# Optimization experiments

Measured on AMD Instinct MI355X. Metric: run time of the kernel, lower is better.

## Reference

```python
import jax, jax.numpy as jnp
import numpy as np

N_USERS = 100000
N_ITEMS = 50000
DIM = 64
HID = 64
E = 3200000
B = 16384


def setup_inputs() -> dict:
    key = jax.random.key(0)
    ks = jax.random.split(key, 16)
    N = N_USERS + N_ITEMS
    return {
        "users": jax.random.randint(ks[0], (B,), 0, N_USERS),
        "items": jax.random.randint(ks[1], (B,), 0, N_ITEMS),
        "edge_index": jax.random.randint(ks[2], (2, E), 0, N),
        "edge_weight": jax.random.uniform(ks[3], (E,), dtype=jnp.float32),
        # learned parameters
        "U": jax.random.normal(ks[4], (N_USERS, DIM), jnp.float32) * 0.1,
        "I": jax.random.normal(ks[5], (N_ITEMS, DIM), jnp.float32) * 0.1,
        "W0": jax.random.normal(ks[6], (DIM, HID), jnp.float32) / np.sqrt(DIM),
        "b0": jnp.zeros((HID,), jnp.float32),
        "g0": jnp.ones((HID,), jnp.float32),
        "be0": jnp.zeros((HID,), jnp.float32),
        "W1": jax.random.normal(ks[7], (HID, HID), jnp.float32) / np.sqrt(HID),
        "b1": jnp.zeros((HID,), jnp.float32),
        "g1": jnp.ones((HID,), jnp.float32),
        "be1": jnp.zeros((HID,), jnp.float32),
        "Wp": jax.random.normal(ks[8], (HID, DIM), jnp.float32) / np.sqrt(HID),
        "bp": jnp.zeros((DIM,), jnp.float32),
        "bu": jnp.zeros((N_USERS,), jnp.float32),
        "bi": jnp.zeros((N_ITEMS,), jnp.float32),
        "mu": jnp.zeros((), jnp.float32),
    }


def _layernorm(h, g, b, eps=1e-5):
    m = jnp.mean(h, axis=-1, keepdims=True)
    v = jnp.mean(jnp.square(h - m), axis=-1, keepdims=True)
    return (h - m) * jax.lax.rsqrt(v + eps) * g + b


def reference(users, items, edge_index, edge_weight, U, I,
              W0, b0, g0, be0, W1, b1, g1, be1, Wp, bp, bu, bi, mu):
    N = U.shape[0] + I.shape[0]
    x = jnp.concatenate([U, I], axis=0)  # [N, DIM]

    # GCN normalization with added self-loops (torch_geometric gcn_norm)
    loop = jnp.arange(N)
    src = jnp.concatenate([edge_index[0], loop])
    dst = jnp.concatenate([edge_index[1], loop])
    ew = jnp.concatenate([edge_weight, jnp.ones((N,), edge_weight.dtype)])
    deg = jax.ops.segment_sum(ew, dst, num_segments=N)
    dinv = jnp.where(deg > 0, jax.lax.rsqrt(deg), 0.0)
    norm = dinv[src] * ew * dinv[dst]  # [E+N]

    def conv(h, W, b):
        hw = h @ W  # [N, HID]
        msgs = norm[:, None] * hw[src]  # gather: [E+N, HID]
        return jax.ops.segment_sum(msgs, dst, num_segments=N) + b

    # layer 0: conv -> layernorm -> relu -> (dropout=identity, eval) -> residual
    h = x
    h_in = h
    h = conv(h, W0, b0)
    h = jax.nn.relu(_layernorm(h, g0, be0)) + h_in
    # layer 1
    h_in = h
    h = conv(h, W1, b1)
    h = jax.nn.relu(_layernorm(h, g1, be1)) + h_in

    h = h @ Wp + bp  # proj_out: [N, DIM]
    h_user = h[:U.shape[0]]
    h_item = h[U.shape[0]:]

    s = jnp.sum(h_user[users] * h_item[items], axis=-1)
    s = s + bu[users] + bi[items] + mu
    return jnp.clip(s, 1.0, 5.0)
```

## Files before the change

kernel.cpp:

```cpp
#include <hip/hip_runtime.h>

#define NU 100000
#define NI 50000
#define NN 150000
#define D  64
#define CAP 47
#define OVF_MAX 4096

#define BINSHIFT 8
#define BINW 256
#define NBINS 586
#define BINCAP 5848
#define STAGE_CAP 12
#define EPT 4
#define SPILL_CAP 262144

typedef unsigned int uint;
typedef unsigned short ushort;

__device__ __forceinline__ float half_reduce_add(float v) {
    #pragma unroll
    for (int m = 16; m >= 1; m >>= 1) v += __shfl_xor(v, m, 64);
    return v;
}
__device__ __forceinline__ ushort f2bf(float f) {
    union { float f; uint i; } c; c.f = f;
    uint r = c.i + 0x7FFF + ((c.i >> 16) & 1);
    return (ushort)(r >> 16);
}
__device__ __forceinline__ float bf2f(ushort u) {
    union { uint i; float f; } c; c.i = ((uint)u) << 16; return c.f;
}
__device__ __forceinline__ float bflo(uint u) {
    return __int_as_float((int)(u << 16));
}
__device__ __forceinline__ float bfhi(uint u) {
    return __int_as_float((int)(u & 0xFFFF0000u));
}
__device__ __forceinline__ uint packbf2(float a, float b) {
    return (uint)f2bf(a) | ((uint)f2bf(b) << 16);
}
__device__ __forceinline__ float lane_bcast(float v, int l) {
    return __int_as_float(__builtin_amdgcn_readlane(__float_as_int(v), l));
}
__device__ __forceinline__ uint enc14(float w) {
    uint b = __float_as_uint(w) + 0x00020000u;
    return b & 0xFFFC0000u;
}
__device__ __forceinline__ float dec14(uint r) {
    return __uint_as_float(r & 0xFFFC0000u);
}
__device__ __forceinline__ uint enc6(float w) {
    int q = (int)(w * 64.0f);
    return (uint)(q < 0 ? 0 : (q > 63 ? 63 : q));
}
__device__ __forceinline__ float dec6(uint q) {
    return ((float)q + 0.5f) * (1.0f / 64.0f);
}
__device__ __forceinline__ void spill_one(int d, uint s, float w,
        uint2* __restrict__ spill, int* __restrict__ spillcnt) {
    int si = atomicAdd(spillcnt, 1);
    if (si < SPILL_CAP) spill[si] = make_uint2(s | enc14(w), (uint)d);
}

__global__ __launch_bounds__(256) void k_bin(
        const int* __restrict__ src, const int* __restrict__ dst,
        const float* __restrict__ ew, int* __restrict__ bincur,
        uint* __restrict__ binbuf, uint2* __restrict__ spill,
        int* __restrict__ spillcnt, int E) {
    __shared__ uint stage[NBINS][STAGE_CAP];
    __shared__ int scnt[NBINS];
    int t = threadIdx.x;
    for (int i = t; i < NBINS; i += 256) scnt[i] = 0;
    __syncthreads();
    const int batch = 256 * EPT;
    for (int base = blockIdx.x * batch; base < E; base += gridDim.x * batch) {
        int dd[EPT]; uint ss[EPT]; float ww[EPT]; int ok[EPT];
        #pragma unroll
        for (int k = 0; k < EPT; ++k) {
            int e = base + k * 256 + t;
            ok[k] = (e < E);
            if (ok[k]) { dd[k] = dst[e]; ss[k] = (uint)src[e]; ww[k] = ew[e]; }
        }
        #pragma unroll
        for (int k = 0; k < EPT; ++k) {
            if (!ok[k]) continue;
            int bin = dd[k] >> BINSHIFT;
            int slot = atomicAdd(&scnt[bin], 1);
            if (slot < STAGE_CAP) {
                stage[bin][slot] = ss[k]
                    | ((uint)(dd[k] & (BINW - 1)) << 18)
                    | (enc6(ww[k]) << 26);
            } else {
                spill_one(dd[k], ss[k], ww[k], spill, spillcnt);
            }
        }
        __syncthreads();
        for (int bin = t; bin < NBINS; bin += 256) {
            int c = scnt[bin]; if (c > STAGE_CAP) c = STAGE_CAP;
            while (c >= 8) {
                int b0 = atomicAdd(&bincur[bin], 8);
                if (b0 + 8 <= BINCAP) {
                    uint4* o4 = (uint4*)(binbuf + (size_t)bin * BINCAP + b0);
                    uint* s1 = &stage[bin][c - 8];
                    o4[0] = make_uint4(s1[0], s1[1], s1[2], s1[3]);
                    o4[1] = make_uint4(s1[4], s1[5], s1[6], s1[7]);
                } else {
                    for (int j = 0; j < 8; ++j) {
                        uint r = stage[bin][c - 8 + j];
                        spill_one((bin << BINSHIFT) + (int)((r >> 18) & 0xFFu),
                                  r & 0x3FFFFu, dec6(r >> 26),
                                  spill, spillcnt);
                    }
                }
                c -= 8;
            }
            scnt[bin] = c;
        }
        __syncthreads();
    }
    for (int bin = t; bin < NBINS; bin += 256) {
        int c = scnt[bin]; if (c > STAGE_CAP) c = STAGE_CAP;
        if (c > 0) {
            int b0 = atomicAdd(&bincur[bin], c);
            for (int j = 0; j < c; ++j) {
                uint r = stage[bin][j];
                if (b0 + j < BINCAP) binbuf[(size_t)bin * BINCAP + b0 + j] = r;
                else spill_one((bin << BINSHIFT) + (int)((r >> 18) & 0xFFu),
                               r & 0x3FFFFu, dec6(r >> 26),
                               spill, spillcnt);
            }
        }
    }
}

__global__ __launch_bounds__(256) void k_regroup(
        const int* __restrict__ bincur, const uint* __restrict__ binbuf,
        const uint2* __restrict__ spill, const int* __restrict__ spillcnt,
        uint* __restrict__ recs, int* __restrict__ cursor,
        float* __restrict__ dinv, int4* __restrict__ ovf,
        int* __restrict__ ovfcnt) {
    __shared__ uint image[256 * CAP];
    __shared__ int cnt[256];
    __shared__ float ovfw[256];
    int t = threadIdx.x;
    int bin = blockIdx.x;
    cnt[t] = 0; ovfw[t] = 0.0f;
    __syncthreads();
    int dbase = bin << BINSHIFT;
    int nrec = bincur[bin]; if (nrec > BINCAP) nrec = BINCAP;
    const uint* bb = binbuf + (size_t)bin * BINCAP;
    for (int i = t; i < nrec; i += 256) {
        uint r = bb[i];
        int dl = (int)((r >> 18) & 0xFFu);
        int slot = atomicAdd(&cnt[dl], 1);
        uint s = r & 0x3FFFFu;
        float w = dec6(r >> 26);
        if (slot < CAP) image[dl * CAP + slot] = enc14(w) | s;
        else {
            atomicAdd(&ovfw[dl], w);
            int o = atomicAdd(ovfcnt, 1);
            if (o < OVF_MAX)
                ovf[o] = make_int4(dbase + dl, (int)s, __float_as_int(w), 0);
        }
    }
    int ns = spillcnt[0]; if (ns > SPILL_CAP) ns = SPILL_CAP;
    for (int i = t; i < ns; i += 256) {
        uint2 e = spill[i];
        int d = (int)e.y;
        if (d < dbase || d >= dbase + BINW) continue;
        int dl = d - dbase;
        int slot = atomicAdd(&cnt[dl], 1);
        if (slot < CAP) image[dl * CAP + slot] = e.x;
        else {
            float w = dec14(e.x);
            atomicAdd(&ovfw[dl], w);
            int o = atomicAdd(ovfcnt, 1);
            if (o < OVF_MAX) ovf[o] = make_int4(d, (int)(e.x & 0x3FFFFu),
                                                __float_as_int(w), 0);
        }
    }
    __syncthreads();
    int ndl = NN - dbase; if (ndl > 256) ndl = 256;
    if (ndl <= 0) return;
    if (t < ndl) {
        int c = cnt[t];
        cursor[dbase + t] = c;
        if (c > CAP) c = CAP;
        float dg = ovfw[t];
        for (int j = 0; j < c; ++j) dg += dec14(image[t * CAP + j]);
        dinv[dbase + t] = rsqrtf(dg + 1.0f);
    }
    int tot = ndl * CAP;
    uint* out = recs + (size_t)dbase * CAP;
    for (int i = t; i < tot; i += 256) out[i] = image[i];
}

__global__ __launch_bounds__(256) void k_gemm(
        const ushort* __restrict__ h, const float* __restrict__ U,
        const float* __restrict__ I, const float* __restrict__ W,
        const float* __restrict__ dinv, ushort* __restrict__ out) {
    int lane = threadIdx.x & 63;
    float wreg[64];
    #pragma unroll
    for (int k = 0; k < 64; ++k) wreg[k] = W[k * 64 + lane];
    int wpb = blockDim.x >> 6;
    int wid = blockIdx.x * wpb + (threadIdx.x >> 6);
    int tw = gridDim.x * wpb;
    for (int n = wid; n < NN; n += tw) {
        float xv;
        if (h) xv = bf2f(h[(size_t)n * D + lane]);
        else   xv = (n < NU) ? U[(size_t)n * D + lane]
                             : I[(size_t)(n - NU) * D + lane];
        float acc = 0.f;
        #pragma unroll
        for (int k = 0; k < 64; ++k)
            acc = fmaf(lane_bcast(xv, k), wreg[k], acc);
        out[(size_t)n * D + lane] = f2bf(acc * dinv[n]);
    }
}

__device__ __forceinline__ float2 conv_accum2(int n, int lane,
        const uint* __restrict__ hw2p, const int* __restrict__ cursor,
        const uint* __restrict__ recs, const int4* __restrict__ ovf,
        const int* __restrict__ ovfcnt) {
    int cnt = __builtin_amdgcn_readfirstlane(cursor[n]);
    if (cnt > CAP) cnt = CAP;
    uint rv = (lane < cnt) ? recs[(size_t)n * CAP + lane] : 0u;
    int odd = lane >> 5;
    int laneoff = lane & 31;
    float ax = 0.f, ay = 0.f;
    int cp = (cnt + 7) & ~7;
    for (int j0 = 0; j0 < cp; j0 += 8) {
        #pragma unroll
        for (int k = 0; k < 4; ++k) {
            uint re = (uint)__builtin_amdgcn_readlane((int)rv, j0 + 2 * k);
            uint ro = (uint)__builtin_amdgcn_readlane((int)rv, j0 + 2 * k + 1);
            uint r  = odd ? ro : re;
            int   s = (int)(r & 0x3FFFFu);
            float w = dec14(r);
            uint x = hw2p[(size_t)s * 32 + laneoff];
            ax = fmaf(w, bflo(x), ax);
            ay = fmaf(w, bfhi(x), ay);
        }
    }
    ax += __shfl_xor(ax, 32, 64);
    ay += __shfl_xor(ay, 32, 64);
    uint xs = hw2p[(size_t)n * 32 + laneoff];
    ax += bflo(xs);
    ay += bfhi(xs);
    int novf = __builtin_amdgcn_readfirstlane(ovfcnt[0]);
    if (novf > 0) {
        if (novf > OVF_MAX) novf = OVF_MAX;
        for (int j = 0; j < novf; ++j) {
            int4 e = ovf[j];
            if (e.x == n) {
                float w = __int_as_float(e.z);
                uint x = hw2p[(size_t)e.y * 32 + laneoff];
                ax = fmaf(w, bflo(x), ax);
                ay = fmaf(w, bfhi(x), ay);
            }
        }
    }
    return make_float2(ax, ay);
}

__device__ __forceinline__ float2 ln_relu2(float2 a, float di, int p,
        const float* __restrict__ b, const float* __restrict__ g,
        const float* __restrict__ be) {
    float2 bb = ((const float2*)b)[p];
    float v0 = fmaf(a.x, di, bb.x);
    float v1 = fmaf(a.y, di, bb.y);
    float m = half_reduce_add(v0 + v1) * (1.0f / 64.0f);
    float d0 = v0 - m, d1 = v1 - m;
    float var = half_reduce_add(d0 * d0 + d1 * d1) * (1.0f / 64.0f);
    float rs = rsqrtf(var + 1e-5f);
    float2 gg = ((const float2*)g)[p];
    float2 ee = ((const float2*)be)[p];
    return make_float2(fmaxf(fmaf(d0 * rs, gg.x, ee.x), 0.0f),
                       fmaxf(fmaf(d1 * rs, gg.y, ee.y), 0.0f));
}

__global__ __launch_bounds__(256) void k_conv1(
        const uint* __restrict__ hw2p, const int* __restrict__ cursor,
        const uint* __restrict__ recs, const int4* __restrict__ ovf,
        const int* __restrict__ ovfcnt, const float* __restrict__ dinv,
        const float* __restrict__ b, const float* __restrict__ g,
        const float* __restrict__ be, const float* __restrict__ U,
        const float* __restrict__ I, uint* __restrict__ out) {
    int lane = threadIdx.x & 63;
    int n = __builtin_amdgcn_readfirstlane(blockIdx.x * 4 + (threadIdx.x >> 6));
    if (n >= NN) return;
    float2 a = conv_accum2(n, lane, hw2p, cursor, recs, ovf, ovfcnt);
    int p = lane & 31;
    float2 y = ln_relu2(a, dinv[n], p, b, g, be);
    const float* R = (n < NU) ? (U + (size_t)n * D) : (I + (size_t)(n - NU) * D);
    float2 rr = ((const float2*)R)[p];
    if (lane < 32)
        out[(size_t)n * 32 + p] = packbf2(y.x + rr.x, y.y + rr.y);
}

__global__ __launch_bounds__(256) void k_conv2score(
        const uint* __restrict__ hw2p, const int* __restrict__ cursor,
        const uint* __restrict__ recs, const int4* __restrict__ ovf,
        const int* __restrict__ ovfcnt, const float* __restrict__ dinv,
        const float* __restrict__ b, const float* __restrict__ g,
        const float* __restrict__ be, const int* __restrict__ users,
        const int* __restrict__ items, const uint* __restrict__ h1u,
        const float* __restrict__ Wp, const float* __restrict__ bp,
        const float* __restrict__ bu, const float* __restrict__ bi,
        const float* __restrict__ mu, float* __restrict__ out, int B) {
    int lane = threadIdx.x & 63;
    float wreg[64];
    #pragma unroll
    for (int k = 0; k < 64; ++k) wreg[k] = Wp[k * 64 + lane];
    float bpl = bp[lane];
    int q = lane & 31;
    int wpb = blockDim.x >> 6;
    int wid = blockIdx.x * wpb + (threadIdx.x >> 6);
    int tw = gridDim.x * wpb;
    for (int p = wid; p < B; p += tw) {
        int un = users[p];
        int in = NU + items[p];
        int nu = __builtin_amdgcn_readfirstlane(un);
        float2 au = conv_accum2(nu, lane, hw2p, cursor, recs, ovf, ovfcnt);
        float2 yu = ln_relu2(au, dinv[nu], q, b, g, be);
        uint ru = h1u[(size_t)nu * 32 + q];
        float2 hu = make_float2(yu.x + bflo(ru), yu.y + bfhi(ru));
        int ni = __builtin_amdgcn_readfirstlane(in);
        float2 ai = conv_accum2(ni, lane, hw2p, cursor, recs, ovf, ovfcnt);
        float2 yi = ln_relu2(ai, dinv[ni], q, b, g, be);
        uint ri = h1u[(size_t)ni * 32 + q];
        float2 hi = make_float2(yi.x + bflo(ri), yi.y + bfhi(ri));
        float pu = bpl, pi = bpl;
        #pragma unroll
        for (int j = 0; j < 32; ++j) {
            pu = fmaf(lane_bcast(hu.x, j), wreg[2 * j], pu);
            pu = fmaf(lane_bcast(hu.y, j), wreg[2 * j + 1], pu);
            pi = fmaf(lane_bcast(hi.x, j), wreg[2 * j], pi);
            pi = fmaf(lane_bcast(hi.y, j), wreg[2 * j + 1], pi);
        }
        float t = pu * pi;
        #pragma unroll
        for (int m = 32; m >= 1; m >>= 1) t += __shfl_xor(t, m, 64);
        if (lane == 0) {
            t += bu[un] + bi[in - NU] + mu[0];
            out[p] = fminf(fmaxf(t, 1.0f), 5.0f);
        }
    }
}

extern "C" void kernel_launch(void* const* d_in, const int* in_sizes, int n_in,
                              void* d_out, int out_size, void* d_ws, size_t ws_size,
                              hipStream_t stream) {
    const int*   users = (const int*)d_in[0];
    const int*   items = (const int*)d_in[1];
    const int*   ei2   = (const int*)d_in[2];
    const float* ew    = (const float*)d_in[3];
    const float* U     = (const float*)d_in[4];
    const float* I     = (const float*)d_in[5];
    const float* W0    = (const float*)d_in[6];
    const float* b0    = (const float*)d_in[7];
    const float* g0    = (const float*)d_in[8];
    const float* be0   = (const float*)d_in[9];
    const float* W1    = (const float*)d_in[10];
    const float* b1    = (const float*)d_in[11];
    const float* g1    = (const float*)d_in[12];
    const float* be1   = (const float*)d_in[13];
    const float* Wp    = (const float*)d_in[14];
    const float* bp    = (const float*)d_in[15];
    const float* bu    = (const float*)d_in[16];
    const float* bi    = (const float*)d_in[17];
    const float* mu    = (const float*)d_in[18];

    int B = in_sizes[0];
    int E = in_sizes[2] / 2;
    const int* srcp = ei2;
    const int* dstp = ei2 + E;

    char* p = (char*)d_ws;
    auto alloc = [&](size_t bytes) -> char* {
        char* r = p;
        p += (bytes + 255) & ~(size_t)255;
        return r;
    };
    int*    cbuf    = (int*)  alloc((size_t)(NBINS + 8) * 4);
    int*    bincur  = cbuf;
    int*    spillcnt= cbuf + NBINS;
    int*    ovfcnt  = cbuf + NBINS + 1;
    int*    cursor  = (int*)  alloc((size_t)NN * 4);
    float*  dinv    = (float*)alloc((size_t)NN * 4);
    int4*   ovf     = (int4*) alloc((size_t)OVF_MAX * 16);
    char*   regA    = alloc((size_t)NN * D * 2 * 2);
    uint*   binbuf  = (uint*) regA;
    uint2*  spill   = (uint2*)(regA + 16 * 1024 * 1024);
    ushort* hw2b    = (ushort*)regA;
    ushort* h1b     = (ushort*)(regA + (size_t)NN * D * 2);
    uint*   recs    = (uint*) alloc((size_t)NN * CAP * 4);
    const uint* hw2p = (const uint*)hw2b;
    const uint* h1u  = (const uint*)h1b;

    hipMemsetAsync(cbuf, 0, (size_t)(NBINS + 8) * 4, stream);

    int gW = (NN + 3) / 4;

    k_bin<<<768, 256, 0, stream>>>(srcp, dstp, ew, bincur, binbuf,
                                   spill, spillcnt, E);
    k_regroup<<<NBINS, 256, 0, stream>>>(bincur, binbuf, spill, spillcnt,
                                         recs, cursor, dinv, ovf, ovfcnt);

    k_gemm<<<2048, 256, 0, stream>>>(nullptr, U, I, W0, dinv, hw2b);
    k_conv1<<<gW, 256, 0, stream>>>(hw2p, cursor, recs, ovf, ovfcnt, dinv,
                                    b0, g0, be0, U, I, (uint*)h1b);
    k_gemm<<<2048, 256, 0, stream>>>(h1b, U, I, W1, dinv, hw2b);
    k_conv2score<<<1024, 256, 0, stream>>>(hw2p, cursor, recs, ovf, ovfcnt, dinv,
                                           b1, g1, be1, users, items, h1u,
                                           Wp, bp, bu, bi, mu,
                                           (float*)d_out, B);
}
```

Before: 421.6 us.

## Fuse layer GEMMs into regroup and conv1 kernels, dropping standalone GEMM launches

The layer-0 transform (x@W0 scaled by dinv) now runs at the end of the regroup kernel, once each bin's dinv values are known. The layer-1 transform (h1@W1 scaled by dinv) now runs inside conv1 on the freshly computed h1 held in registers. This removes two kernel launches and the re-read of h1 from global memory. It costs extra registers for the weight row in the regroup and conv1 kernels, which may lower occupancy, and it needs separate msg1/msg2 buffers, which changes the workspace layout including where the spill region starts.

```diff
diff --git a/kernel.cpp b/kernel.cpp
--- a/kernel.cpp
+++ b/kernel.cpp
@@ -27,9 +27,6 @@
     union { float f; uint i; } c; c.f = f;
     uint r = c.i + 0x7FFF + ((c.i >> 16) & 1);
     return (ushort)(r >> 16);
-}
-__device__ __forceinline__ float bf2f(ushort u) {
-    union { uint i; float f; } c; c.i = ((uint)u) << 16; return c.f;
 }
 __device__ __forceinline__ float bflo(uint u) {
     return __int_as_float((int)(u << 16));
@@ -134,16 +131,23 @@
     }
 }
 
-__global__ __launch_bounds__(256) void k_regroup(
+__global__ __launch_bounds__(256) void k_regroupg(
         const int* __restrict__ bincur, const uint* __restrict__ binbuf,
         const uint2* __restrict__ spill, const int* __restrict__ spillcnt,
         uint* __restrict__ recs, int* __restrict__ cursor,
         float* __restrict__ dinv, int4* __restrict__ ovf,
-        int* __restrict__ ovfcnt) {
+        int* __restrict__ ovfcnt, const float* __restrict__ U,
+        const float* __restrict__ I, const float* __restrict__ W0,
+        ushort* __restrict__ msg1) {
     __shared__ uint image[256 * CAP];
     __shared__ int cnt[256];
     __shared__ float ovfw[256];
+    __shared__ float sdinv[256];
     int t = threadIdx.x;
+    int lane = t & 63;
+    float wreg[64];
+    #pragma unroll
+    for (int k = 0; k < 64; ++k) wreg[k] = W0[k * 64 + lane];
     int bin = blockIdx.x;
     cnt[t] = 0; ovfw[t] = 0.0f;
     __syncthreads();
@@ -189,34 +193,24 @@
         if (c > CAP) c = CAP;
         float dg = ovfw[t];
         for (int j = 0; j < c; ++j) dg += dec14(image[t * CAP + j]);
-        dinv[dbase + t] = rsqrtf(dg + 1.0f);
-    }
+        float di = rsqrtf(dg + 1.0f);
+        dinv[dbase + t] = di;
+        sdinv[t] = di;
+    }
+    __syncthreads();
     int tot = ndl * CAP;
     uint* out = recs + (size_t)dbase * CAP;
     for (int i = t; i < tot; i += 256) out[i] = image[i];
-}
-
-__global__ __launch_bounds__(256) void k_gemm(
-        const ushort* __restrict__ h, const float* __restrict__ U,
-        const float* __restrict__ I, const float* __restrict__ W,
-        const float* __restrict__ dinv, ushort* __restrict__ out) {
-    int lane = threadIdx.x & 63;
-    float wreg[64];
-    #pragma unroll
-    for (int k = 0; k < 64; ++k) wreg[k] = W[k * 64 + lane];
-    int wpb = blockDim.x >> 6;
-    int wid = blockIdx.x * wpb + (threadIdx.x >> 6);
-    int tw = gridDim.x * wpb;
-    for (int n = wid; n < NN; n += tw) {
-        float xv;
-        if (h) xv = bf2f(h[(size_t)n * D + lane]);
-        else   xv = (n < NU) ? U[(size_t)n * D + lane]
-                             : I[(size_t)(n - NU) * D + lane];
+    int wv = t >> 6;
+    for (int i = wv; i < ndl; i += 4) {
+        int n = dbase + i;
+        float xv = (n < NU) ? U[(size_t)n * D + lane]
+                            : I[(size_t)(n - NU) * D + lane];
         float acc = 0.f;
         #pragma unroll
         for (int k = 0; k < 64; ++k)
             acc = fmaf(lane_bcast(xv, k), wreg[k], acc);
-        out[(size_t)n * D + lane] = f2bf(acc * dinv[n]);
+        msg1[(size_t)n * D + lane] = f2bf(acc * sdinv[i]);
     }
 }
 
@@ -281,27 +275,45 @@
                        fmaxf(fmaf(d1 * rs, gg.y, ee.y), 0.0f));
 }
 
-__global__ __launch_bounds__(256) void k_conv1(
-        const uint* __restrict__ hw2p, const int* __restrict__ cursor,
+__global__ __launch_bounds__(256) void k_conv1g(
+        const uint* __restrict__ msg1p, const int* __restrict__ cursor,
         const uint* __restrict__ recs, const int4* __restrict__ ovf,
         const int* __restrict__ ovfcnt, const float* __restrict__ dinv,
         const float* __restrict__ b, const float* __restrict__ g,
         const float* __restrict__ be, const float* __restrict__ U,
-        const float* __restrict__ I, uint* __restrict__ out) {
+        const float* __restrict__ I, const float* __restrict__ W1,
+        uint* __restrict__ h1out, ushort* __restrict__ msg2) {
     int lane = threadIdx.x & 63;
-    int n = __builtin_amdgcn_readfirstlane(blockIdx.x * 4 + (threadIdx.x >> 6));
-    if (n >= NN) return;
-    float2 a = conv_accum2(n, lane, hw2p, cursor, recs, ovf, ovfcnt);
+    float wreg[64];
+    #pragma unroll
+    for (int k = 0; k < 64; ++k) wreg[k] = W1[k * 64 + lane];
+    int wpb = blockDim.x >> 6;
+    int wid = blockIdx.x * wpb + (threadIdx.x >> 6);
+    int tw = gridDim.x * wpb;
     int p = lane & 31;
-    float2 y = ln_relu2(a, dinv[n], p, b, g, be);
-    const float* R = (n < NU) ? (U + (size_t)n * D) : (I + (size_t)(n - NU) * D);
-    float2 rr = ((const float2*)R)[p];
-    if (lane < 32)
-        out[(size_t)n * 32 + p] = packbf2(y.x + rr.x, y.y + rr.y);
+    for (int n0 = wid; n0 < NN; n0 += tw) {
+        int n = __builtin_amdgcn_readfirstlane(n0);
+        float2 a = conv_accum2(n, lane, msg1p, cursor, recs, ovf, ovfcnt);
+        float di = dinv[n];
+        float2 y = ln_relu2(a, di, p, b, g, be);
+        const float* R = (n < NU) ? (U + (size_t)n * D)
+                                  : (I + (size_t)(n - NU) * D);
+        float2 rr = ((const float2*)R)[p];
+        float2 h = make_float2(y.x + rr.x, y.y + rr.y);
+        if (lane < 32)
+            h1out[(size_t)n * 32 + p] = packbf2(h.x, h.y);
+        float acc = 0.f;
+        #pragma unroll
+        for (int j = 0; j < 32; ++j) {
+            acc = fmaf(lane_bcast(h.x, j), wreg[2 * j], acc);
+            acc = fmaf(lane_bcast(h.y, j), wreg[2 * j + 1], acc);
+        }
+        msg2[(size_t)n * D + lane] = f2bf(acc * di);
+    }
 }
 
 __global__ __launch_bounds__(256) void k_conv2score(
-        const uint* __restrict__ hw2p, const int* __restrict__ cursor,
+        const uint* __restrict__ msg2p, const int* __restrict__ cursor,
         const uint* __restrict__ recs, const int4* __restrict__ ovf,
         const int* __restrict__ ovfcnt, const float* __restrict__ dinv,
         const float* __restrict__ b, const float* __restrict__ g,
@@ -323,12 +335,12 @@
         int un = users[p];
         int in = NU + items[p];
         int nu = __builtin_amdgcn_readfirstlane(un);
-        float2 au = conv_accum2(nu, lane, hw2p, cursor, recs, ovf, ovfcnt);
+        float2 au = conv_accum2(nu, lane, msg2p, cursor, recs, ovf, ovfcnt);
         float2 yu = ln_relu2(au, dinv[nu], q, b, g, be);
         uint ru = h1u[(size_t)nu * 32 + q];
         float2 hu = make_float2(yu.x + bflo(ru), yu.y + bfhi(ru));
         int ni = __builtin_amdgcn_readfirstlane(in);
-        float2 ai = conv_accum2(ni, lane, hw2p, cursor, recs, ovf, ovfcnt);
+        float2 ai = conv_accum2(ni, lane, msg2p, cursor, recs, ovf, ovfcnt);
         float2 yi = ln_relu2(ai, dinv[ni], q, b, g, be);
         uint ri = h1u[(size_t)ni * 32 + q];
         float2 hi = make_float2(yi.x + bflo(ri), yi.y + bfhi(ri));
@@ -391,29 +403,28 @@
     int*    cursor  = (int*)  alloc((size_t)NN * 4);
     float*  dinv    = (float*)alloc((size_t)NN * 4);
     int4*   ovf     = (int4*) alloc((size_t)OVF_MAX * 16);
-    char*   regA    = alloc((size_t)NN * D * 2 * 2);
+    char*   regA    = alloc((size_t)NN * D * 2);
     uint*   binbuf  = (uint*) regA;
-    uint2*  spill   = (uint2*)(regA + 16 * 1024 * 1024);
-    ushort* hw2b    = (ushort*)regA;
-    ushort* h1b     = (ushort*)(regA + (size_t)NN * D * 2);
+    uint2*  spill   = (uint2*)(regA + 14 * 1024 * 1024);
+    ushort* h1b     = (ushort*)regA;
+    ushort* msg1    = (ushort*)alloc((size_t)NN * D * 2);
+    ushort* msg2    = (ushort*)alloc((size_t)NN * D * 2);
     uint*   recs    = (uint*) alloc((size_t)NN * CAP * 4);
-    const uint* hw2p = (const uint*)hw2b;
-    const uint* h1u  = (const uint*)h1b;
+    const uint* msg1p = (const uint*)msg1;
+    const uint* msg2p = (const uint*)msg2;
+    const uint* h1u   = (const uint*)h1b;
 
     hipMemsetAsync(cbuf, 0, (size_t)(NBINS + 8) * 4, stream);
-
-    int gW = (NN + 3) / 4;
 
     k_bin<<<768, 256, 0, stream>>>(srcp, dstp, ew, bincur, binbuf,
                                    spill, spillcnt, E);
-    k_regroup<<<NBINS, 256, 0, stream>>>(bincur, binbuf, spill, spillcnt,
-                                         recs, cursor, dinv, ovf, ovfcnt);
-
-    k_gemm<<<2048, 256, 0, stream>>>(nullptr, U, I, W0, dinv, hw2b);
-    k_conv1<<<gW, 256, 0, stream>>>(hw2p, cursor, recs, ovf, ovfcnt, dinv,
-                                    b0, g0, be0, U, I, (uint*)h1b);
-    k_gemm<<<2048, 256, 0, stream>>>(h1b, U, I, W1, dinv, hw2b);
-    k_conv2score<<<1024, 256, 0, stream>>>(hw2p, cursor, recs, ovf, ovfcnt, dinv,
+    k_regroupg<<<NBINS, 256, 0, stream>>>(bincur, binbuf, spill, spillcnt,
+                                          recs, cursor, dinv, ovf, ovfcnt,
+                                          U, I, W0, msg1);
+    k_conv1g<<<2048, 256, 0, stream>>>(msg1p, cursor, recs, ovf, ovfcnt, dinv,
+                                       b0, g0, be0, U, I, W1,
+                                       (uint*)h1b, msg2);
+    k_conv2score<<<1024, 256, 0, stream>>>(msg2p, cursor, recs, ovf, ovfcnt, dinv,
                                            b1, g1, be1, users, items, h1u,
                                            Wp, bp, bu, bi, mu,
                                            (float*)d_out, B);
```

Measured after the change: 452.3 us. +7.3%, slower.
